# Kernel optimization log

Hardware: AMD Instinct MI355X
Metric: run time of the kernel (lower is better)

The kernel has to match this reference:

```python
import jax, jax.numpy as jnp
import numpy as np

BATCH = 64
INPUT_LENGTH = 128
N_TERMINALS = 64
N_NONTERMINALS = 128


def setup_inputs() -> dict:
    key = jax.random.key(0)
    k1, k2, k3 = jax.random.split(key, 3)
    input_tensor = jax.random.uniform(k1, (BATCH, INPUT_LENGTH, N_TERMINALS), dtype=jnp.float32)
    terminal_productions = jax.random.normal(k2, (N_NONTERMINALS, N_TERMINALS), dtype=jnp.float32)
    nonterminal_productions = jax.random.normal(k3, (N_NONTERMINALS, N_NONTERMINALS, N_TERMINALS), dtype=jnp.float32)
    return {
        "input_tensor": input_tensor,
        "terminal_productions": terminal_productions,
        "nonterminal_productions": nonterminal_productions,
    }


def reference(input_tensor, terminal_productions, nonterminal_productions):
    # input_tensor: [B, L, T]
    tp = jax.nn.sigmoid(terminal_productions)            # [N, T]
    ntp = jax.nn.sigmoid(nonterminal_productions)        # [N, N, T]

    # step 0: terminal production choices
    tpc = jnp.einsum('nt,bt->bn', tp, input_tensor[:, 0])  # [B, N]
    out0 = tpc[:, 0]                                        # [B]

    def step(carry, x_i):
        prev_choices, prev_out = carry                     # [B, N], [B]
        # per-batch nonterminal production choice matrix: [B, N, N]
        npc = jnp.clip(jnp.einsum('nmt,bt->bnm', ntp, x_i), 0.0, 1.0)
        cur = jnp.clip(jnp.einsum('bnm,bm->bn', npc, prev_choices), 0.0, 1.0)
        mask = x_i[:, N_TERMINALS - 1]                     # [B]
        out = prev_out * mask + cur[:, 0] * (1.0 - mask)
        return (cur, out), None

    xs = jnp.swapaxes(input_tensor[:, 1:], 0, 1)           # [L-1, B, T]
    (final_choices, final_out), _ = jax.lax.scan(step, (tpc, out0), xs)
    return final_out[:, None]                              # [B, 1]
```

## Files before the change

kernel.cpp:

```cpp
#include <hip/hip_runtime.h>
#include <hip/hip_bf16.h>

typedef unsigned int u32;
typedef unsigned char u8;
typedef _Float16 f16;
typedef f16 f16x2 __attribute__((ext_vector_type(2)));
typedef short s16x8 __attribute__((ext_vector_type(8)));
typedef float f32x4 __attribute__((ext_vector_type(4)));

#define BB 64
#define LL 128
#define TT 64
#define NN 128
#define NM (NN*NN)

__device__ __forceinline__ float sigf(float v) {
    return 1.0f / (1.0f + __expf(-v));
}

__device__ __forceinline__ float clip01(float v) {
    return fminf(fmaxf(v, 0.f), 1.f);
}

__device__ __forceinline__ u32 f2bf(float f) {
    u32 u = __builtin_bit_cast(u32, f);
    return (u + 0x7fffu + ((u >> 16) & 1u)) >> 16;
}

__device__ __forceinline__ float fdot2f(f16x2 wa, f16x2 xa, float ca) {
#if defined(__HIP_DEVICE_COMPILE__) && __has_builtin(__builtin_amdgcn_fdot2)
    return __builtin_amdgcn_fdot2(wa, xa, ca, false);
#else
    return ca + (float)wa[0] * (float)xa[0] + (float)wa[1] * (float)xa[1];
#endif
}

__device__ __forceinline__ u32 ud4(u32 a, u32 b, u32 c) {
#if defined(__HIP_DEVICE_COMPILE__) && __has_builtin(__builtin_amdgcn_udot4)
    return __builtin_amdgcn_udot4(a, b, c, false);
#else
    return c + (a & 255u) * (b & 255u) + ((a >> 8) & 255u) * ((b >> 8) & 255u)
             + ((a >> 16) & 255u) * ((b >> 16) & 255u) + (a >> 24) * (b >> 24);
#endif
}

__global__ __launch_bounds__(256) void pack_w(const float* __restrict__ ntp,
                                              ushort* __restrict__ wpk) {
    const int g = blockIdx.x * 256 + threadIdx.x;
    const int l = g & 63, h = (g >> 6) & 1, i = g >> 7;
    const int row = i * 16 + (l & 15);
    const int t0 = h * 32 + ((l >> 4) << 3);
    const float* src = ntp + row * 64 + t0;
    float4 f0 = *reinterpret_cast<const float4*>(src);
    float4 f1 = *reinterpret_cast<const float4*>(src + 4);
    float v[8] = {f0.x, f0.y, f0.z, f0.w, f1.x, f1.y, f1.z, f1.w};
    u32 o[4];
    #pragma unroll
    for (int q = 0; q < 4; ++q)
        o[q] = f2bf(sigf(v[2 * q])) | (f2bf(sigf(v[2 * q + 1])) << 16);
    uint4 ov; ov.x = o[0]; ov.y = o[1]; ov.z = o[2]; ov.w = o[3];
    *reinterpret_cast<uint4*>(wpk + (size_t)g * 8) = ov;
}

__global__ __launch_bounds__(256) void pack_x(const float* __restrict__ x_all,
                                              ushort* __restrict__ xpk) {
    const int g = blockIdx.x * 256 + threadIdx.x;
    const int l = g & 63, h = (g >> 6) & 1, j = (g >> 7) & 7, b = g >> 10;
    const int s = j * 16 + (l & 15);
    const int t0 = h * 32 + ((l >> 4) << 3);
    const float* src = x_all + ((size_t)b * LL + s) * TT + t0;
    float4 f0 = *reinterpret_cast<const float4*>(src);
    float4 f1 = *reinterpret_cast<const float4*>(src + 4);
    float v[8] = {f0.x, f0.y, f0.z, f0.w, f1.x, f1.y, f1.z, f1.w};
    u32 o[4];
    #pragma unroll
    for (int q = 0; q < 4; ++q)
        o[q] = f2bf(v[2 * q]) | (f2bf(v[2 * q + 1]) << 16);
    uint4 ov; ov.x = o[0]; ov.y = o[1]; ov.z = o[2]; ov.w = o[3];
    *reinterpret_cast<uint4*>(xpk + (size_t)g * 8) = ov;
}

__global__ __launch_bounds__(256) void gemm_mfma(const ushort* __restrict__ wpk,
                                                 const ushort* __restrict__ xpk,
                                                 u8* __restrict__ npc) {
    __shared__ __align__(16) u8 stg[4][16384];
    const int b = blockIdx.x >> 4;
    const int nb = blockIdx.x & 15;
    const int wv = threadIdx.x >> 6, l = threadIdx.x & 63;

    uint4 xf[8][2];
    #pragma unroll
    for (int j = 0; j < 8; ++j)
        #pragma unroll
        for (int h = 0; h < 2; ++h)
            xf[j][h] = *reinterpret_cast<const uint4*>(
                xpk + (size_t)(((b * 8 + j) * 2 + h) * 64 + l) * 8);

    const int c = l & 15, r0 = (l >> 4) * 4;
    u8* stw = stg[wv];
    const int khi  = (nb >> 3) * 8;
    const int nlow = (nb & 7) * 8;

    for (int mg2 = 0; mg2 < 2; ++mg2) {
        const int mg = wv * 2 + mg2;
        #pragma unroll
        for (int n_l = 0; n_l < 8; ++n_l) {
            const int i = (nb * 8 + n_l) * 8 + mg;
            uint4 a0 = *reinterpret_cast<const uint4*>(wpk + (size_t)((i * 2 + 0) * 64 + l) * 8);
            uint4 a1 = *reinterpret_cast<const uint4*>(wpk + (size_t)((i * 2 + 1) * 64 + l) * 8);
            const f32x4 z = {0.f, 0.f, 0.f, 0.f};
            f32x4 acc[8];
            #pragma unroll
            for (int j = 0; j < 8; ++j)
                acc[j] = __builtin_amdgcn_mfma_f32_16x16x32_bf16(
                    __builtin_bit_cast(s16x8, a0), __builtin_bit_cast(s16x8, xf[j][0]), z, 0, 0, 0);
            #pragma unroll
            for (int j = 0; j < 8; ++j)
                acc[j] = __builtin_amdgcn_mfma_f32_16x16x32_bf16(
                    __builtin_bit_cast(s16x8, a1), __builtin_bit_cast(s16x8, xf[j][1]), acc[j], 0, 0, 0);

            const int sk = (((n_l + c) & 7) << 4) + r0;
            #pragma unroll
            for (int j = 0; j < 8; ++j) {
                u32 w = 0;
                #pragma unroll
                for (int r = 0; r < 4; ++r) {
                    float q = clip01(acc[j][r]) * 255.f + 0.5f;
                    w |= ((u32)q) << (8 * r);
                }
                *reinterpret_cast<u32*>(stw + j * 2048 + c * 128 + sk) = w;
            }
        }
        asm volatile("s_waitcnt lgkmcnt(0)" ::: "memory");
        __builtin_amdgcn_sched_barrier(0);

        const int nr = l & 7;
        #pragma unroll
        for (int j = 0; j < 8; ++j) {
            #pragma unroll
            for (int half = 0; half < 2; ++half) {
                const int cc = half * 8 + (l >> 3);
                uint4 v = *reinterpret_cast<const uint4*>(
                    stw + j * 2048 + cc * 128 + (((nr + cc) & 7) << 4));
                *reinterpret_cast<uint4*>(npc + ((size_t)b << 21) + ((size_t)j << 18)
                    + ((size_t)cc << 14) + ((size_t)(mg + khi) << 10)
                    + ((nlow + nr) << 4)) = v;
            }
        }
        asm volatile("s_waitcnt lgkmcnt(0)" ::: "memory");
        __builtin_amdgcn_sched_barrier(0);
    }
}

__global__ __launch_bounds__(64, 1) void recur6(const float* __restrict__ x_all,
                                                const float* __restrict__ tp,
                                                const u8* __restrict__ npc,
                                                float* __restrict__ outp) {
    __shared__ __align__(16) u8 prev_lds[2][128];
    __shared__ float masks_lds[128];
    __shared__ float tpc_lds[128];
    __shared__ float x0_lds[64];

    const int b = blockIdx.x, l = threadIdx.x;
    const u8* npcl = npc + ((size_t)b << 21) + ((size_t)l << 4);

    x0_lds[l] = x_all[(size_t)b * 8192 + l];
    masks_lds[l]      = x_all[(size_t)b * 8192 + l * 64 + 63];
    masks_lds[64 + l] = x_all[(size_t)b * 8192 + (64 + l) * 64 + 63];
    asm volatile("s_waitcnt lgkmcnt(0)" ::: "memory");
    __builtin_amdgcn_sched_barrier(0);

#define LOADSET(R, T) do { \
        int _t = (T) <= 127 ? (T) : 127; \
        const u8* _p = npcl + ((size_t)(_t >> 4) << 18) + ((size_t)(_t & 15) << 14); \
        _Pragma("unroll") \
        for (int _k = 0; _k < 16; ++_k) \
            R[_k] = *reinterpret_cast<const uint4*>(_p + _k * 1024); \
        asm volatile("" ::: "memory"); \
        __builtin_amdgcn_sched_barrier(0); \
    } while (0)

    uint4 nA[16], nB[16], nC[16], nD[16];
    LOADSET(nA, 1); LOADSET(nB, 2); LOADSET(nC, 3); LOADSET(nD, 4);

    float a0 = 0.f, a1 = 0.f;
    #pragma unroll
    for (int t4 = 0; t4 < 16; ++t4) {
        float4 xv = *reinterpret_cast<const float4*>(x0_lds + t4 * 4);
        float4 w0 = *reinterpret_cast<const float4*>(tp + l * 64 + t4 * 4);
        float4 w1 = *reinterpret_cast<const float4*>(tp + (64 + l) * 64 + t4 * 4);
        a0 += sigf(w0.x) * xv.x; a0 += sigf(w0.y) * xv.y;
        a0 += sigf(w0.z) * xv.z; a0 += sigf(w0.w) * xv.w;
        a1 += sigf(w1.x) * xv.x; a1 += sigf(w1.y) * xv.y;
        a1 += sigf(w1.z) * xv.z; a1 += sigf(w1.w) * xv.w;
    }
    tpc_lds[l] = a0; tpc_lds[64 + l] = a1;
    float out_r = a0;
    asm volatile("s_waitcnt lgkmcnt(0)" ::: "memory");
    __builtin_amdgcn_sched_barrier(0);

    {
        float s0f = 0.f, s1f = 0.f;
        #pragma unroll
        for (int k = 0; k < 8; ++k) {
            u32 ax[4] = {nA[k].x, nA[k].y, nA[k].z, nA[k].w};
            u32 bx[4] = {nA[k + 8].x, nA[k + 8].y, nA[k + 8].z, nA[k + 8].w};
            #pragma unroll
            for (int w = 0; w < 4; ++w) {
                float4 tv = *reinterpret_cast<const float4*>(tpc_lds + k * 16 + w * 4);
                u32 aw = ax[w], bw = bx[w];
                s0f += (float)(aw & 255u) * tv.x + (float)((aw >> 8) & 255u) * tv.y
                     + (float)((aw >> 16) & 255u) * tv.z + (float)(aw >> 24) * tv.w;
                s1f += (float)(bw & 255u) * tv.x + (float)((bw >> 8) & 255u) * tv.y
                     + (float)((bw >> 16) & 255u) * tv.z + (float)(bw >> 24) * tv.w;
            }
        }
        float c0 = clip01(s0f * (1.f / 255.f));
        float c1 = clip01(s1f * (1.f / 255.f));
        float mk = masks_lds[1];
        if (l == 0) out_r = out_r * mk + c0 * (1.f - mk);
        prev_lds[0][l]      = (u8)(c0 * 255.f + 0.5f);
        prev_lds[0][64 + l] = (u8)(c1 * 255.f + 0.5f);
        asm volatile("s_waitcnt lgkmcnt(0)" ::: "memory");
        __builtin_amdgcn_sched_barrier(0);
    }
    LOADSET(nA, 5);

    int p = 0;

#define STEP(R, S) do { \
        uint4 pv[8]; \
        _Pragma("unroll") \
        for (int _q = 0; _q < 8; ++_q) \
            pv[_q] = *reinterpret_cast<const uint4*>(&prev_lds[p][_q * 16]); \
        float mk = masks_lds[(S)]; \
        u32 s0 = 0, t0 = 0, s1 = 0, t1 = 0; \
        _Pragma("unroll") \
        for (int _k = 0; _k < 4; ++_k) { \
            s0 = ud4(R[_k].x, pv[_k].x, s0); s0 = ud4(R[_k].y, pv[_k].y, s0); \
            s0 = ud4(R[_k].z, pv[_k].z, s0); s0 = ud4(R[_k].w, pv[_k].w, s0); \
        } \
        _Pragma("unroll") \
        for (int _k = 4; _k < 8; ++_k) { \
            t0 = ud4(R[_k].x, pv[_k].x, t0); t0 = ud4(R[_k].y, pv[_k].y, t0); \
            t0 = ud4(R[_k].z, pv[_k].z, t0); t0 = ud4(R[_k].w, pv[_k].w, t0); \
        } \
        _Pragma("unroll") \
        for (int _k = 8; _k < 12; ++_k) { \
            s1 = ud4(R[_k].x, pv[_k - 8].x, s1); s1 = ud4(R[_k].y, pv[_k - 8].y, s1); \
            s1 = ud4(R[_k].z, pv[_k - 8].z, s1); s1 = ud4(R[_k].w, pv[_k - 8].w, s1); \
        } \
        _Pragma("unroll") \
        for (int _k = 12; _k < 16; ++_k) { \
            t1 = ud4(R[_k].x, pv[_k - 8].x, t1); t1 = ud4(R[_k].y, pv[_k - 8].y, t1); \
            t1 = ud4(R[_k].z, pv[_k - 8].z, t1); t1 = ud4(R[_k].w, pv[_k - 8].w, t1); \
        } \
        float c0 = fminf((float)(s0 + t0) * (1.f / 65025.f), 1.f); \
        float c1 = fminf((float)(s1 + t1) * (1.f / 65025.f), 1.f); \
        u32 q0 = (u32)(c0 * 255.f + 0.5f), q1 = (u32)(c1 * 255.f + 0.5f); \
        if (l == 0) out_r = out_r * mk + c0 * (1.f - mk); \
        prev_lds[p ^ 1][l]      = (u8)q0; \
        prev_lds[p ^ 1][64 + l] = (u8)q1; \
        asm volatile("s_waitcnt lgkmcnt(0)" ::: "memory"); \
        __builtin_amdgcn_sched_barrier(0); \
        p ^= 1; \
    } while (0)

    for (int g = 0; g < 31; ++g) {
        const int s = 2 + 4 * g;
        STEP(nB, s);     LOADSET(nB, s + 4);
        STEP(nC, s + 1); LOADSET(nC, s + 5);
        STEP(nD, s + 2); LOADSET(nD, s + 6);
        STEP(nA, s + 3); LOADSET(nA, s + 7);
    }
    STEP(nB, 126);
    STEP(nC, 127);

#undef STEP
#undef LOADSET

    if (l == 0) outp[b] = out_r;
}

__global__ __launch_bounds__(256) void sig_transpose(const float* __restrict__ ntp,
                                                     u32* __restrict__ out) {
    __shared__ float lds[64 * 65];
    const int nm0 = blockIdx.x * 64;
    const int tid = threadIdx.x;
    #pragma unroll
    for (int it = 0; it < 16; ++it) {
        int idx = it * 256 + tid;
        int r = idx >> 6, c = idx & 63;
        lds[r * 65 + c] = sigf(ntp[(nm0 + r) * 64 + c]);
    }
    __syncthreads();
    #pragma unroll
    for (int it = 0; it < 8; ++it) {
        int o = it * 256 + tid;
        int tpi = o >> 6, r = o & 63;
        f16x2 h;
        h[0] = (f16)lds[r * 65 + 2 * tpi];
        h[1] = (f16)lds[r * 65 + 2 * tpi + 1];
        out[tpi * NM + nm0 + r] = __builtin_bit_cast(u32, h);
    }
}

__global__ __launch_bounds__(1024) void grammar_fused(
    const float* __restrict__ x_all,
    const float* __restrict__ tp,
    const u32*  __restrict__ ntpT2,
    float* __restrict__ outp) {
    __shared__ float x_lds[LL * TT];
    __shared__ float prevbuf[2][NN];
    __shared__ u32 x2_lds[2][32];

    const int b = blockIdx.x;
    const int tid = threadIdx.x;
    const int lane16 = tid & 15;
    const int g = tid >> 4;
    const int mbase = lane16 * 8;

    const float* xb = x_all + b * (LL * TT);
    #pragma unroll
    for (int it = 0; it < 8; ++it) {
        int idx = it * 1024 + tid;
        x_lds[idx] = xb[idx];
    }
    __syncthreads();

    if (tid < NN) {
        float acc = 0.f;
        #pragma unroll 8
        for (int t = 0; t < TT; ++t)
            acc += sigf(tp[tid * TT + t]) * x_lds[t];
        prevbuf[0][tid] = acc;
    }
    __syncthreads();
    float out_r = 0.f;
    if (tid == 0) out_r = prevbuf[0][0];

    int p = 0;
    for (int i0 = 1; i0 < LL; i0 += 2) {
        const int ns = (LL - i0) >= 2 ? 2 : 1;
        if (tid < 64) {
            int s = tid >> 5, tpi = tid & 31;
            f16x2 h;
            if (s < ns) {
                h[0] = (f16)x_lds[(i0 + s) * TT + 2 * tpi];
                h[1] = (f16)x_lds[(i0 + s) * TT + 2 * tpi + 1];
            } else {
                h[0] = (f16)0.f; h[1] = (f16)0.f;
            }
            x2_lds[s][tpi] = __builtin_bit_cast(u32, h);
        }
        __syncthreads();

        float acc[2][2][8];
        #pragma unroll
        for (int k = 0; k < 2; ++k)
            #pragma unroll
            for (int s = 0; s < 2; ++s)
                #pragma unroll
                for (int j = 0; j < 8; ++j) acc[k][s][j] = 0.f;

        #pragma unroll 2
        for (int tpi = 0; tpi < 32; ++tpi) {
            f16x2 xv0 = __builtin_bit_cast(f16x2, x2_lds[0][tpi]);
            f16x2 xv1 = __builtin_bit_cast(f16x2, x2_lds[1][tpi]);
            const u32* base = ntpT2 + tpi * NM + 8 * tid;
            #pragma unroll
            for (int k = 0; k < 2; ++k) {
                uint4 w0 = *reinterpret_cast<const uint4*>(base + 8192 * k);
                uint4 w1 = *reinterpret_cast<const uint4*>(base + 8192 * k + 4);
                u32 wv[8] = {w0.x, w0.y, w0.z, w0.w, w1.x, w1.y, w1.z, w1.w};
                #pragma unroll
                for (int j = 0; j < 8; ++j) {
                    f16x2 w = __builtin_bit_cast(f16x2, wv[j]);
                    acc[k][0][j] = fdot2f(w, xv0, acc[k][0][j]);
                    acc[k][1][j] = fdot2f(w, xv1, acc[k][1][j]);
                }
            }
        }

        for (int s = 0; s < ns; ++s) {
            float4 pv0 = *reinterpret_cast<const float4*>(&prevbuf[p][mbase]);
            float4 pv1 = *reinterpret_cast<const float4*>(&prevbuf[p][mbase + 4]);
            float pvv[8] = {pv0.x, pv0.y, pv0.z, pv0.w, pv1.x, pv1.y, pv1.z, pv1.w};
            #pragma unroll
            for (int k = 0; k < 2; ++k) {
                float part = 0.f;
                #pragma unroll
                for (int j = 0; j < 8; ++j) {
                    float npcv = clip01(acc[k][s][j]);
                    part += npcv * pvv[j];
                }
                part += __shfl_xor(part, 1);
                part += __shfl_xor(part, 2);
                part += __shfl_xor(part, 4);
                part += __shfl_xor(part, 8);
                if (lane16 == 0) {
                    float c = clip01(part);
                    prevbuf[p ^ 1][g + 64 * k] = c;
                    if (tid == 0 && k == 0) {
                        float mask = x_lds[(i0 + s) * TT + 63];
                        out_r = out_r * mask + c * (1.f - mask);
                    }
                }
            }
            p ^= 1;
            __syncthreads();
        }
    }

    if (tid == 0) outp[b] = out_r;
}

extern "C" void kernel_launch(void* const* d_in, const int* in_sizes, int n_in,
                              void* d_out, int out_size, void* d_ws, size_t ws_size,
                              hipStream_t stream) {
    const float* input_tensor = (const float*)d_in[0];
    const float* term_prod    = (const float*)d_in[1];
    const float* nonterm_prod = (const float*)d_in[2];
    float* outp = (float*)d_out;

    const size_t MB = 1024 * 1024;
    const size_t NPC_BYTES = 128 * MB;
    const size_t WPK_BYTES = 2 * MB;
    const size_t XPK_BYTES = 1 * MB;

    if (ws_size >= NPC_BYTES + WPK_BYTES + XPK_BYTES + MB) {
        u8* npcbuf  = (u8*)d_ws;
        ushort* wpk = (ushort*)((char*)d_ws + NPC_BYTES);
        ushort* xpk = (ushort*)((char*)d_ws + NPC_BYTES + WPK_BYTES);
        pack_w<<<512, 256, 0, stream>>>(nonterm_prod, wpk);
        pack_x<<<256, 256, 0, stream>>>(input_tensor, xpk);
        gemm_mfma<<<1024, 256, 0, stream>>>(wpk, xpk, npcbuf);
        recur6<<<BB, 64, 0, stream>>>(input_tensor, term_prod, npcbuf, outp);
    } else {
        u32* ntpT2 = (u32*)d_ws;
        sig_transpose<<<256, 256, 0, stream>>>(nonterm_prod, ntpT2);
        grammar_fused<<<BB, 1024, 0, stream>>>(input_tensor, term_prod, ntpT2, outp);
    }
}
```

Before: 95.12 us.

## Split recurrence kernel across 256 threads with pairwise shuffle reduction

```diff
diff --git a/kernel.cpp b/kernel.cpp
--- a/kernel.cpp
+++ b/kernel.cpp
@@ -152,116 +152,105 @@
     }
 }
 
-__global__ __launch_bounds__(64, 1) void recur6(const float* __restrict__ x_all,
-                                                const float* __restrict__ tp,
-                                                const u8* __restrict__ npc,
-                                                float* __restrict__ outp) {
-    __shared__ __align__(16) u8 prev_lds[2][128];
-    __shared__ float masks_lds[128];
-    __shared__ float tpc_lds[128];
-    __shared__ float x0_lds[64];
-
-    const int b = blockIdx.x, l = threadIdx.x;
-    const u8* npcl = npc + ((size_t)b << 21) + ((size_t)l << 4);
-
-    x0_lds[l] = x_all[(size_t)b * 8192 + l];
-    masks_lds[l]      = x_all[(size_t)b * 8192 + l * 64 + 63];
-    masks_lds[64 + l] = x_all[(size_t)b * 8192 + (64 + l) * 64 + 63];
-    asm volatile("s_waitcnt lgkmcnt(0)" ::: "memory");
-    __builtin_amdgcn_sched_barrier(0);
+__global__ __launch_bounds__(256, 1) void recur8(const float* __restrict__ x_all,
+                                                 const float* __restrict__ tp,
+                                                 const u8* __restrict__ npc,
+                                                 float* __restrict__ outp) {
+    __shared__ __align__(16) u8 prev_lds[2][NN];
+    __shared__ float masks_lds[LL];
+    __shared__ float tpc_lds[NN];
+    __shared__ float x0_lds[TT];
+
+    const int b = blockIdx.x, tid = threadIdx.x;
+    const int n = tid >> 1, h = tid & 1;
+    const int koff = (n >> 6) * 8 + h * 4;
+    const u8* npcl = npc + ((size_t)b << 21) + (u32)koff * 1024 + (u32)(n & 63) * 16;
+
+    if (tid < 128) masks_lds[tid] = x_all[(size_t)b * 8192 + tid * 64 + 63];
+    else if (tid < 192) x0_lds[tid - 128] = x_all[(size_t)b * 8192 + (tid - 128)];
+    __syncthreads();
 
 #define LOADSET(R, T) do { \
         int _t = (T) <= 127 ? (T) : 127; \
         const u8* _p = npcl + ((size_t)(_t >> 4) << 18) + ((size_t)(_t & 15) << 14); \
+        R[0] = *reinterpret_cast<const uint4*>(_p); \
+        R[1] = *reinterpret_cast<const uint4*>(_p + 1024); \
+        R[2] = *reinterpret_cast<const uint4*>(_p + 2048); \
+        R[3] = *reinterpret_cast<const uint4*>(_p + 3072); \
+        asm volatile("" ::: "memory"); \
+    } while (0)
+
+    uint4 nA[4], nB[4], nC[4], nD[4];
+    LOADSET(nA, 1); LOADSET(nB, 2); LOADSET(nC, 3); LOADSET(nD, 4);
+
+    float out_r = 0.f;
+    if (tid < 128) {
+        float a = 0.f;
+        #pragma unroll
+        for (int t4 = 0; t4 < 16; ++t4) {
+            float4 xv = *reinterpret_cast<const float4*>(x0_lds + t4 * 4);
+            float4 w0 = *reinterpret_cast<const float4*>(tp + tid * 64 + t4 * 4);
+            a += sigf(w0.x) * xv.x; a += sigf(w0.y) * xv.y;
+            a += sigf(w0.z) * xv.z; a += sigf(w0.w) * xv.w;
+        }
+        tpc_lds[tid] = a;
+        if (tid == 0) out_r = a;
+    }
+    asm volatile("s_waitcnt lgkmcnt(0)" ::: "memory");
+    __builtin_amdgcn_s_barrier();
+    __builtin_amdgcn_sched_barrier(0);
+
+    {
+        float sf = 0.f;
+        #pragma unroll
+        for (int j = 0; j < 4; ++j) {
+            u32 cw[4] = {nA[j].x, nA[j].y, nA[j].z, nA[j].w};
+            #pragma unroll
+            for (int w = 0; w < 4; ++w) {
+                float4 tv = *reinterpret_cast<const float4*>(
+                    tpc_lds + h * 64 + j * 16 + w * 4);
+                u32 aw = cw[w];
+                sf += (float)(aw & 255u) * tv.x + (float)((aw >> 8) & 255u) * tv.y
+                    + (float)((aw >> 16) & 255u) * tv.z + (float)(aw >> 24) * tv.w;
+            }
+        }
+        float tot = sf + __shfl_xor(sf, 1);
+        float c0 = clip01(tot * (1.f / 255.f));
+        if (h == 0) prev_lds[0][n] = (u8)(c0 * 255.f + 0.5f);
+        if (tid == 0) {
+            float mk = masks_lds[1];
+            out_r = out_r * mk + c0 * (1.f - mk);
+        }
+        asm volatile("s_waitcnt lgkmcnt(0)" ::: "memory");
+        __builtin_amdgcn_s_barrier();
+        __builtin_amdgcn_sched_barrier(0);
+    }
+    LOADSET(nA, 5);
+
+    int p = 0;
+
+#define STEP(R, S) do { \
+        uint4 pv[4]; \
         _Pragma("unroll") \
-        for (int _k = 0; _k < 16; ++_k) \
-            R[_k] = *reinterpret_cast<const uint4*>(_p + _k * 1024); \
-        asm volatile("" ::: "memory"); \
-        __builtin_amdgcn_sched_barrier(0); \
-    } while (0)
-
-    uint4 nA[16], nB[16], nC[16], nD[16];
-    LOADSET(nA, 1); LOADSET(nB, 2); LOADSET(nC, 3); LOADSET(nD, 4);
-
-    float a0 = 0.f, a1 = 0.f;
-    #pragma unroll
-    for (int t4 = 0; t4 < 16; ++t4) {
-        float4 xv = *reinterpret_cast<const float4*>(x0_lds + t4 * 4);
-        float4 w0 = *reinterpret_cast<const float4*>(tp + l * 64 + t4 * 4);
-        float4 w1 = *reinterpret_cast<const float4*>(tp + (64 + l) * 64 + t4 * 4);
-        a0 += sigf(w0.x) * xv.x; a0 += sigf(w0.y) * xv.y;
-        a0 += sigf(w0.z) * xv.z; a0 += sigf(w0.w) * xv.w;
-        a1 += sigf(w1.x) * xv.x; a1 += sigf(w1.y) * xv.y;
-        a1 += sigf(w1.z) * xv.z; a1 += sigf(w1.w) * xv.w;
-    }
-    tpc_lds[l] = a0; tpc_lds[64 + l] = a1;
-    float out_r = a0;
-    asm volatile("s_waitcnt lgkmcnt(0)" ::: "memory");
-    __builtin_amdgcn_sched_barrier(0);
-
-    {
-        float s0f = 0.f, s1f = 0.f;
-        #pragma unroll
-        for (int k = 0; k < 8; ++k) {
-            u32 ax[4] = {nA[k].x, nA[k].y, nA[k].z, nA[k].w};
-            u32 bx[4] = {nA[k + 8].x, nA[k + 8].y, nA[k + 8].z, nA[k + 8].w};
-            #pragma unroll
-            for (int w = 0; w < 4; ++w) {
-                float4 tv = *reinterpret_cast<const float4*>(tpc_lds + k * 16 + w * 4);
-                u32 aw = ax[w], bw = bx[w];
-                s0f += (float)(aw & 255u) * tv.x + (float)((aw >> 8) & 255u) * tv.y
-                     + (float)((aw >> 16) & 255u) * tv.z + (float)(aw >> 24) * tv.w;
-                s1f += (float)(bw & 255u) * tv.x + (float)((bw >> 8) & 255u) * tv.y
-                     + (float)((bw >> 16) & 255u) * tv.z + (float)(bw >> 24) * tv.w;
-            }
-        }
-        float c0 = clip01(s0f * (1.f / 255.f));
-        float c1 = clip01(s1f * (1.f / 255.f));
-        float mk = masks_lds[1];
-        if (l == 0) out_r = out_r * mk + c0 * (1.f - mk);
-        prev_lds[0][l]      = (u8)(c0 * 255.f + 0.5f);
-        prev_lds[0][64 + l] = (u8)(c1 * 255.f + 0.5f);
-        asm volatile("s_waitcnt lgkmcnt(0)" ::: "memory");
-        __builtin_amdgcn_sched_barrier(0);
-    }
-    LOADSET(nA, 5);
-
-    int p = 0;
-
-#define STEP(R, S) do { \
-        uint4 pv[8]; \
-        _Pragma("unroll") \
-        for (int _q = 0; _q < 8; ++_q) \
-            pv[_q] = *reinterpret_cast<const uint4*>(&prev_lds[p][_q * 16]); \
+        for (int _q = 0; _q < 4; ++_q) \
+            pv[_q] = *reinterpret_cast<const uint4*>(&prev_lds[p][h * 64 + _q * 16]); \
         float mk = masks_lds[(S)]; \
-        u32 s0 = 0, t0 = 0, s1 = 0, t1 = 0; \
-        _Pragma("unroll") \
-        for (int _k = 0; _k < 4; ++_k) { \
-            s0 = ud4(R[_k].x, pv[_k].x, s0); s0 = ud4(R[_k].y, pv[_k].y, s0); \
-            s0 = ud4(R[_k].z, pv[_k].z, s0); s0 = ud4(R[_k].w, pv[_k].w, s0); \
-        } \
-        _Pragma("unroll") \
-        for (int _k = 4; _k < 8; ++_k) { \
-            t0 = ud4(R[_k].x, pv[_k].x, t0); t0 = ud4(R[_k].y, pv[_k].y, t0); \
-            t0 = ud4(R[_k].z, pv[_k].z, t0); t0 = ud4(R[_k].w, pv[_k].w, t0); \
-        } \
-        _Pragma("unroll") \
-        for (int _k = 8; _k < 12; ++_k) { \
-            s1 = ud4(R[_k].x, pv[_k - 8].x, s1); s1 = ud4(R[_k].y, pv[_k - 8].y, s1); \
-            s1 = ud4(R[_k].z, pv[_k - 8].z, s1); s1 = ud4(R[_k].w, pv[_k - 8].w, s1); \
-        } \
-        _Pragma("unroll") \
-        for (int _k = 12; _k < 16; ++_k) { \
-            t1 = ud4(R[_k].x, pv[_k - 8].x, t1); t1 = ud4(R[_k].y, pv[_k - 8].y, t1); \
-            t1 = ud4(R[_k].z, pv[_k - 8].z, t1); t1 = ud4(R[_k].w, pv[_k - 8].w, t1); \
-        } \
-        float c0 = fminf((float)(s0 + t0) * (1.f / 65025.f), 1.f); \
-        float c1 = fminf((float)(s1 + t1) * (1.f / 65025.f), 1.f); \
-        u32 q0 = (u32)(c0 * 255.f + 0.5f), q1 = (u32)(c1 * 255.f + 0.5f); \
-        if (l == 0) out_r = out_r * mk + c0 * (1.f - mk); \
-        prev_lds[p ^ 1][l]      = (u8)q0; \
-        prev_lds[p ^ 1][64 + l] = (u8)q1; \
+        u32 s0 = 0, s1 = 0; \
+        s0 = ud4(R[0].x, pv[0].x, s0); s0 = ud4(R[0].y, pv[0].y, s0); \
+        s0 = ud4(R[0].z, pv[0].z, s0); s0 = ud4(R[0].w, pv[0].w, s0); \
+        s1 = ud4(R[1].x, pv[1].x, s1); s1 = ud4(R[1].y, pv[1].y, s1); \
+        s1 = ud4(R[1].z, pv[1].z, s1); s1 = ud4(R[1].w, pv[1].w, s1); \
+        s0 = ud4(R[2].x, pv[2].x, s0); s0 = ud4(R[2].y, pv[2].y, s0); \
+        s0 = ud4(R[2].z, pv[2].z, s0); s0 = ud4(R[2].w, pv[2].w, s0); \
+        s1 = ud4(R[3].x, pv[3].x, s1); s1 = ud4(R[3].y, pv[3].y, s1); \
+        s1 = ud4(R[3].z, pv[3].z, s1); s1 = ud4(R[3].w, pv[3].w, s1); \
+        float sf = (float)(s0 + s1); \
+        float tot = sf + __shfl_xor(sf, 1); \
+        float c0 = fminf(tot * (1.f / 65025.f), 1.f); \
+        if (h == 0) prev_lds[p ^ 1][n] = (u8)(c0 * 255.f + 0.5f); \
+        if (tid == 0) out_r = out_r * mk + c0 * (1.f - mk); \
         asm volatile("s_waitcnt lgkmcnt(0)" ::: "memory"); \
+        __builtin_amdgcn_s_barrier(); \
         __builtin_amdgcn_sched_barrier(0); \
         p ^= 1; \
     } while (0)
@@ -279,7 +268,7 @@
 #undef STEP
 #undef LOADSET
 
-    if (l == 0) outp[b] = out_r;
+    if (tid == 0) outp[b] = out_r;
 }
 
 __global__ __launch_bounds__(256) void sig_transpose(const float* __restrict__ ntp,
@@ -435,7 +424,7 @@
         pack_w<<<512, 256, 0, stream>>>(nonterm_prod, wpk);
         pack_x<<<256, 256, 0, stream>>>(input_tensor, xpk);
         gemm_mfma<<<1024, 256, 0, stream>>>(wpk, xpk, npcbuf);
-        recur6<<<BB, 64, 0, stream>>>(input_tensor, term_prod, npcbuf, outp);
+        recur8<<<BB, 256, 0, stream>>>(input_tensor, term_prod, npcbuf, outp);
     } else {
         u32* ntpT2 = (u32*)d_ws;
         sig_transpose<<<256, 256, 0, stream>>>(nonterm_prod, ntpT2);
```

Result: faster. 81.12 us (-14.7%).
